# Optimization experiments

Hardware: AMD Instinct MI355X
Metric: run time of the kernel (lower is better)

The kernel has to match this reference:

```python
import jax, jax.numpy as jnp
import numpy as np

B = 64        # graphs per batch
NP = 96       # nodes per graph
H = 64        # hid_size
IN_F = 32     # node feature dim
E_F = 16      # edge feature dim
DEG = 8       # avg degree
ENSEMBLE = 1


def _lin(key, fan_in, fan_out):
    return jax.random.normal(key, (fan_in, fan_out), jnp.float32) / np.float32(np.sqrt(fan_in))


def setup_inputs() -> dict:
    key = jax.random.key(0)
    ks = jax.random.split(key, 12)
    N = B * NP
    E = B * NP * DEG
    x = jax.random.normal(ks[0], (N, IN_F), jnp.float32)
    edge_attr = jax.random.normal(ks[1], (E, E_F), jnp.float32)
    # within-graph random edges (sorted per-graph blocks, like is_sorted=True)
    rng = np.random.default_rng(0)
    off = (np.arange(B) * NP)[:, None]
    src = (rng.integers(0, NP, size=(B, NP * DEG)) + off).ravel()
    dst = (rng.integers(0, NP, size=(B, NP * DEG)) + off).ravel()
    edge_index = jnp.asarray(np.stack([src, dst]), dtype=jnp.int32)
    # idx = concat of triu_indices(n, -n) per graph == ALL n^2 pairs per graph
    tri = np.triu_indices(NP, -NP)
    idx0 = jnp.asarray((tri[0][None, :] + off).ravel(), jnp.int32)  # [B*NP^2]
    idx1 = jnp.asarray((tri[1][None, :] + off).ravel(), jnp.int32)
    params = dict(
        W_atom=_lin(ks[2], IN_F, H), b_atom=jnp.zeros((H,), jnp.float32),
        W_bond=_lin(ks[3], E_F, H), b_bond=jnp.zeros((H,), jnp.float32),
        W_node=_lin(ks[4], H, H), b_node=jnp.zeros((H,), jnp.float32),
        W_edge=_lin(ks[5], H, H), b_edge=jnp.zeros((H,), jnp.float32),
        W1=_lin(ks[6], 3 * H, H), b1=jnp.zeros((H,), jnp.float32),
        W2=_lin(ks[7], H, H), b2=jnp.zeros((H,), jnp.float32),
        W3=_lin(ks[8], H, ENSEMBLE), b3=jnp.zeros((ENSEMBLE,), jnp.float32),
    )
    return dict(x=x, edge_attr=edge_attr, edge_index=edge_index,
                idx0=idx0, idx1=idx1, n=NP, **params)


def reference(x, edge_attr, edge_index, idx0, idx1, n,
              W_atom, b_atom, W_bond, b_bond, W_node, b_node,
              W_edge, b_edge, W1, b1, W2, b2, W3, b3):
    # encoders
    xh = x @ W_atom + b_atom                 # [N, H]
    eh = edge_attr @ W_bond + b_bond         # [E, H]
    emb_n = xh @ W_node + b_node             # [N, H]
    emb_e = eh @ W_edge + b_edge             # [E, H]
    # SparseTensor.to_dense() then gather at idx == scatter-add edge embeddings
    # into the per-graph dense pairwise slot (duplicates sum, missing = 0),
    # without materializing the O(N^2) adjacency.
    u, v = edge_index[0], edge_index[1]
    g = u // n
    pair_idx = g * (n * n) + (u - g * n) * n + (v - g * n)   # [E]
    P = idx0.shape[0]                         # B * n^2, idx enumerates all pairs row-major
    pair_e = jnp.zeros((P, emb_e.shape[1]), emb_e.dtype).at[pair_idx].add(emb_e)
    emb = jnp.concatenate((emb_n[idx0], emb_n[idx1], pair_e), axis=-1)  # [P, 3H]
    # MLP [3H, H, H, ensemble], plain last layer
    h = jax.nn.relu(emb @ W1 + b1)
    h = jax.nn.relu(h @ W2 + b2)
    return h @ W3 + b3                        # [P, ensemble]
```

## Files before the change

### kernel.cpp

```cpp
#include <hip/hip_runtime.h>

#define NPG 96
#define BGR 64
#define HID 64
#define INF 32
#define EF  16
#define DEG 8
#define NN  (BGR*NPG)
#define NE  (BGR*NPG*DEG)
#define EPG (NPG*DEG)
#define PPG (NPG*NPG)
#define BMW 288

typedef short bf16x8 __attribute__((ext_vector_type(8)));
typedef float f32x4  __attribute__((ext_vector_type(4)));

__device__ __forceinline__ unsigned rne2(float lo, float hi) {
    union { float f; unsigned u; } a, b; a.f = lo; b.f = hi;
    unsigned ua = a.u + 0x7FFF + ((a.u >> 16) & 1);
    unsigned ub = b.u + 0x7FFF + ((b.u >> 16) & 1);
    return (ua >> 16) | (ub & 0xFFFF0000u);
}
__device__ __forceinline__ unsigned short rne1(float x) {
    union { float f; unsigned u; } a; a.f = x;
    return (unsigned short)((a.u + 0x7FFF + ((a.u >> 16) & 1)) >> 16);
}

__global__ __launch_bounds__(768) void prep_kernel(
    const float* __restrict__ x,
    const float* __restrict__ W_atom, const float* __restrict__ b_atom,
    const float* __restrict__ W_node, const float* __restrict__ b_node,
    const float* __restrict__ W1,     const float* __restrict__ b1,
    const float* __restrict__ ea,     const int* __restrict__ eidx,
    const float* __restrict__ W_bond, const float* __restrict__ b_bond,
    const float* __restrict__ W_edge, const float* __restrict__ b_edge,
    float* __restrict__ Abuf, float* __restrict__ Bbuf,
    int* __restrict__ fkey, int* __restrict__ fcnt,
    float* __restrict__ fsea, int* __restrict__ gcount,
    float* __restrict__ wec, float* __restrict__ biascg,
    unsigned* __restrict__ gbm)
{
    __shared__ __align__(16) char smem[45504];
    const int t = threadIdx.x;

    if (blockIdx.x >= 64) {
        float* sh = (float*)smem;
        const int wave = t >> 6, lane = t & 63;
        const int n = __builtin_amdgcn_readfirstlane((blockIdx.x - 64)*12 + wave);
        const float* xr = x + n * INF;

        float xh = b_atom[lane];
        #pragma unroll
        for (int k = 0; k < INF; ++k) xh += xr[k] * W_atom[k*HID + lane];
        sh[wave*64 + lane] = xh;
        __syncthreads();

        float en = b_node[lane];
        #pragma unroll
        for (int k = 0; k < HID; ++k) en += sh[wave*64 + k] * W_node[k*HID + lane];
        __syncthreads();
        sh[wave*64 + lane] = en;
        __syncthreads();

        float a = b1[lane], b = 0.f;
        #pragma unroll
        for (int k = 0; k < HID; ++k) {
            const float ek = sh[wave*64 + k];
            a += ek * W1[k*HID + lane];
            b += ek * W1[(HID + k)*HID + lane];
        }
        Abuf[n*HID + lane] = a;
        Bbuf[n*HID + lane] = b;
        return;
    }

    int*      head = (int*)smem;
    int*      nxt  = (int*)(smem + 36864);
    float*    sU   = (float*)(smem + 36864 + 3072);
    float*    sbe  = (float*)(smem + 36864 + 3072 + 4096);
    unsigned* bm   = (unsigned*)(smem + 36864+3072+4096+256);
    int*      lcnt = (int*)(smem + 36864+3072+4096+256+1152);
    const int g = blockIdx.x;

    for (int idx = t; idx < PPG; idx += EPG) head[idx] = -1;
    for (int idx = t; idx < BMW; idx += EPG) bm[idx] = 0u;
    if (t == 0) *lcnt = 0;

    const int u = eidx[g*EPG + t]      - g*NPG;
    const int v = eidx[NE + g*EPG + t] - g*NPG;
    const int key = u*NPG + v;
    __syncthreads();

    nxt[t] = atomicExch(&head[key], t);
    __syncthreads();

    if (head[key] == t) {
        const float* eag = ea + (size_t)g * EPG * EF;
        float s[EF];
        #pragma unroll
        for (int q = 0; q < EF; ++q) s[q] = 0.f;
        int cnt = 0;
        for (int e = t; e != -1; e = nxt[e]) {
            ++cnt;
            const float4* p = (const float4*)(eag + e*EF);
            #pragma unroll
            for (int q4 = 0; q4 < 4; ++q4) {
                const float4 f = p[q4];
                s[q4*4+0] += f.x; s[q4*4+1] += f.y;
                s[q4*4+2] += f.z; s[q4*4+3] += f.w;
            }
        }
        atomicOr(&bm[key >> 5], 1u << (key & 31));
        const int pos  = atomicAdd(lcnt, 1);
        const int slot = g*EPG + pos;
        fkey[slot] = key;
        fcnt[slot] = cnt;
        #pragma unroll
        for (int q = 0; q < EF; ++q) fsea[slot*EF + q] = s[q];
    }
    __syncthreads();
    for (int idx = t; idx < BMW; idx += EPG) gbm[g*BMW + idx] = bm[idx];
    if (t == 0) gcount[g] = *lcnt;

    if (g == 0) {
        for (int idx = t; idx < 16*64; idx += EPG) {
            const int r = idx >> 6, c = idx & 63;
            float s = 0.f;
            for (int k = 0; k < 64; ++k) s += W_bond[r*64+k] * W_edge[k*64+c];
            sU[idx] = s;
        }
        if (t < 64) {
            float s2 = b_edge[t];
            for (int k = 0; k < 64; ++k) s2 += b_bond[k] * W_edge[k*64+t];
            sbe[t] = s2;
        }
        __syncthreads();
        for (int idx = t; idx < 16*64; idx += EPG) {
            const int r = idx >> 6, c = idx & 63;
            float s = 0.f;
            for (int k = 0; k < 64; ++k) s += sU[r*64+k] * W1[(128+k)*64+c];
            wec[idx] = s;
        }
        if (t < 64) {
            float sc = 0.f;
            for (int k = 0; k < 64; ++k) sc += sbe[k] * W1[(128+k)*64+t];
            biascg[t] = sc;
        }
    }
}

#define SBST 68
#define W2ST 72
#define FIXW 16
__global__ __launch_bounds__(256) void pair_kernel(
    const float* __restrict__ Abuf, const float* __restrict__ Bbuf,
    const int* __restrict__ fkey, const int* __restrict__ fcnt,
    const float* __restrict__ fsea, const int* __restrict__ gcount,
    const float* __restrict__ wec,  const float* __restrict__ biascg,
    const unsigned* __restrict__ gbm,
    const float* __restrict__ W2,   const float* __restrict__ b2,
    const float* __restrict__ W3,   const float* __restrict__ b3,
    float* __restrict__ out)
{
    __shared__ __align__(16) char smem[37504];
    const int t = threadIdx.x;
    const int wave = t >> 6, lane = t & 63;
    const int col = lane & 15, q = lane >> 4;
    const float b3v = b3[0];

    if (blockIdx.x < 768) {
        float*          sB   = (float*)smem;
        float*          sA   = (float*)(smem + 26112);
        unsigned short* sW2t = (unsigned short*)(smem + 28160);
        unsigned*       sBM  = (unsigned*)(smem + 28160 + 9216);
        const int g  = blockIdx.x / 12;
        const int i0 = (blockIdx.x % 12) * 8;

        const float* Bg = Bbuf + g * NPG * 64;
        for (int idx = t; idx < NPG*64; idx += 256)
            sB[(idx >> 6)*SBST + (idx & 63)] = Bg[idx];
        for (int idx = t; idx < 8*64; idx += 256)
            sA[idx] = Abuf[(g*NPG + i0 + (idx >> 6))*64 + (idx & 63)];
        for (int idx = t; idx < 64*64; idx += 256) {
            const int k = idx >> 6, n = idx & 63;
            sW2t[n*W2ST + k] = rne1(W2[idx]);
        }
        if (t < 24) sBM[t] = gbm[g*BMW + i0*3 + t];
        __syncthreads();

        bf16x8 w2f[4][2];
        #pragma unroll
        for (int nt = 0; nt < 4; ++nt)
            #pragma unroll
            for (int c = 0; c < 2; ++c)
                w2f[nt][c] = *(const bf16x8*)(sW2t + (nt*16 + col)*W2ST + c*32 + q*8);

        float w3l[4], b2l[4];
        #pragma unroll
        for (int nt = 0; nt < 4; ++nt) {
            w3l[nt] = W3[nt*16 + col];
            b2l[nt] = b2[nt*16 + col];
        }

        #pragma unroll
        for (int ii = 0; ii < 2; ++ii) {
            const int il = wave*2 + ii;
            float areg[16];
            {
                const float4* Ar = (const float4*)(sA + il*64 + q*8);
                const float4 a0 = Ar[0], a1 = Ar[1];
                const float4 a2 = Ar[8], a3 = Ar[9];
                areg[0]=a0.x; areg[1]=a0.y; areg[2]=a0.z; areg[3]=a0.w;
                areg[4]=a1.x; areg[5]=a1.y; areg[6]=a1.z; areg[7]=a1.w;
                areg[8]=a2.x; areg[9]=a2.y; areg[10]=a2.z; areg[11]=a2.w;
                areg[12]=a3.x; areg[13]=a3.y; areg[14]=a3.z; areg[15]=a3.w;
            }
            float* outr = out + g*PPG + (i0 + il)*NPG;

            for (int jc = 0; jc < 6; ++jc) {
                const int j0 = jc * 16;
                union { bf16x8 v; unsigned u[4]; } h1[2];
                const float* Brow = sB + (j0 + col)*SBST + q*8;
                #pragma unroll
                for (int c = 0; c < 2; ++c) {
                    const float4 b0 = *(const float4*)(Brow + c*32);
                    const float4 b1v = *(const float4*)(Brow + c*32 + 4);
                    float h[8];
                    h[0] = fmaxf(areg[c*8+0] + b0.x, 0.f);
                    h[1] = fmaxf(areg[c*8+1] + b0.y, 0.f);
                    h[2] = fmaxf(areg[c*8+2] + b0.z, 0.f);
                    h[3] = fmaxf(areg[c*8+3] + b0.w, 0.f);
                    h[4] = fmaxf(areg[c*8+4] + b1v.x, 0.f);
                    h[5] = fmaxf(areg[c*8+5] + b1v.y, 0.f);
                    h[6] = fmaxf(areg[c*8+6] + b1v.z, 0.f);
                    h[7] = fmaxf(areg[c*8+7] + b1v.w, 0.f);
                    #pragma unroll
                    for (int p2 = 0; p2 < 4; ++p2)
                        h1[c].u[p2] = rne2(h[2*p2], h[2*p2+1]);
                }
                f32x4 acc[4];
                #pragma unroll
                for (int nt = 0; nt < 4; ++nt) {
                    f32x4 z = {0.f, 0.f, 0.f, 0.f};
                    z = __builtin_amdgcn_mfma_f32_16x16x32_bf16(h1[0].v, w2f[nt][0], z, 0, 0, 0);
                    z = __builtin_amdgcn_mfma_f32_16x16x32_bf16(h1[1].v, w2f[nt][1], z, 0, 0, 0);
                    acc[nt] = z;
                }
                float p[4];
                #pragma unroll
                for (int r = 0; r < 4; ++r) {
                    float s = 0.f;
                    #pragma unroll
                    for (int nt = 0; nt < 4; ++nt)
                        s += fmaxf(acc[nt][r] + b2l[nt], 0.f) * w3l[nt];
                    p[r] = s;
                }
                #pragma unroll
                for (int off = 1; off < 16; off <<= 1) {
                    #pragma unroll
                    for (int r = 0; r < 4; ++r)
                        p[r] += __shfl_xor(p[r], off, 64);
                }
                if (col == 0) {
                    #pragma unroll
                    for (int r = 0; r < 4; ++r) {
                        const int j = j0 + q*4 + r;
                        if (!((sBM[il*3 + (j >> 5)] >> (j & 31)) & 1u))
                            outr[j] = p[r] + b3v;
                    }
                }
            }
        }
        return;
    }

    unsigned short* sW2t = (unsigned short*)smem;
    float*          sWEc = (float*)(smem + 9216);
    float*          sbc  = (float*)(smem + 9216 + 4096);

    for (int idx = t; idx < 64*64; idx += 256) {
        const int k = idx >> 6, n = idx & 63;
        sW2t[n*W2ST + k] = rne1(W2[idx]);
    }
    for (int idx = t; idx < 16*64; idx += 256) sWEc[idx] = wec[idx];
    if (t < 64) sbc[t] = biascg[t];
    __syncthreads();

    const int fb = blockIdx.x - 768;
    const int s0 = (fb * 4 + wave) * FIXW;
    const int g  = s0 / EPG;
    const int l0 = s0 % EPG;
    const int cg = gcount[g];
    if (l0 >= cg) return;

    bf16x8 w2f[4][2];
    #pragma unroll
    for (int nt = 0; nt < 4; ++nt)
        #pragma unroll
        for (int c = 0; c < 2; ++c)
            w2f[nt][c] = *(const bf16x8*)(sW2t + (nt*16 + col)*W2ST + c*32 + q*8);

    float w3l[4], b2l[4];
    #pragma unroll
    for (int nt = 0; nt < 4; ++nt) {
        w3l[nt] = W3[nt*16 + col];
        b2l[nt] = b2[nt*16 + col];
    }
    const int k0 = q * 8;

    union { bf16x8 v; unsigned u[4]; } h1[2];
    #pragma unroll
    for (int p2 = 0; p2 < 4; ++p2) { h1[0].u[p2] = 0; h1[1].u[p2] = 0; }

    const int s = s0 + col;
    if (l0 + col < cg) {
        const int key  = fkey[s];
        const float cf = (float)fcnt[s];
        const int ui = key / NPG, vi = key % NPG;

        float se[16];
        {
            const float4* p = (const float4*)(fsea + (size_t)s * EF);
            #pragma unroll
            for (int q4 = 0; q4 < 4; ++q4) {
                const float4 f = p[q4];
                se[q4*4+0] = f.x; se[q4*4+1] = f.y;
                se[q4*4+2] = f.z; se[q4*4+3] = f.w;
            }
        }

        float ck[16];
        #pragma unroll
        for (int kk = 0; kk < 8; ++kk) {
            ck[kk]     = cf * sbc[k0 + kk];
            ck[8 + kk] = cf * sbc[32 + k0 + kk];
        }
        #pragma unroll
        for (int qq = 0; qq < 16; ++qq) {
            const float sq = se[qq];
            const float4 w0 = *(const float4*)(sWEc + qq*64 + k0);
            const float4 w1 = *(const float4*)(sWEc + qq*64 + k0 + 4);
            const float4 w2v = *(const float4*)(sWEc + qq*64 + k0 + 32);
            const float4 w3v = *(const float4*)(sWEc + qq*64 + k0 + 36);
            ck[0]  += sq * w0.x;  ck[1]  += sq * w0.y;
            ck[2]  += sq * w0.z;  ck[3]  += sq * w0.w;
            ck[4]  += sq * w1.x;  ck[5]  += sq * w1.y;
            ck[6]  += sq * w1.z;  ck[7]  += sq * w1.w;
            ck[8]  += sq * w2v.x; ck[9]  += sq * w2v.y;
            ck[10] += sq * w2v.z; ck[11] += sq * w2v.w;
            ck[12] += sq * w3v.x; ck[13] += sq * w3v.y;
            ck[14] += sq * w3v.z; ck[15] += sq * w3v.w;
        }

        const float* Ar = Abuf + (g*NPG + ui)*64;
        const float* Br = Bbuf + (g*NPG + vi)*64;
        const float4 a0 = *(const float4*)(Ar + k0);
        const float4 a1 = *(const float4*)(Ar + k0 + 4);
        const float4 a2 = *(const float4*)(Ar + k0 + 32);
        const float4 a3 = *(const float4*)(Ar + k0 + 36);
        const float4 c0 = *(const float4*)(Br + k0);
        const float4 c1 = *(const float4*)(Br + k0 + 4);
        const float4 c2 = *(const float4*)(Br + k0 + 32);
        const float4 c3 = *(const float4*)(Br + k0 + 36);

        float h[16];
        h[0]  = fmaxf(a0.x + c0.x + ck[0],  0.f);
        h[1]  = fmaxf(a0.y + c0.y + ck[1],  0.f);
        h[2]  = fmaxf(a0.z + c0.z + ck[2],  0.f);
        h[3]  = fmaxf(a0.w + c0.w + ck[3],  0.f);
        h[4]  = fmaxf(a1.x + c1.x + ck[4],  0.f);
        h[5]  = fmaxf(a1.y + c1.y + ck[5],  0.f);
        h[6]  = fmaxf(a1.z + c1.z + ck[6],  0.f);
        h[7]  = fmaxf(a1.w + c1.w + ck[7],  0.f);
        h[8]  = fmaxf(a2.x + c2.x + ck[8],  0.f);
        h[9]  = fmaxf(a2.y + c2.y + ck[9],  0.f);
        h[10] = fmaxf(a2.z + c2.z + ck[10], 0.f);
        h[11] = fmaxf(a2.w + c2.w + ck[11], 0.f);
        h[12] = fmaxf(a3.x + c3.x + ck[12], 0.f);
        h[13] = fmaxf(a3.y + c3.y + ck[13], 0.f);
        h[14] = fmaxf(a3.z + c3.z + ck[14], 0.f);
        h[15] = fmaxf(a3.w + c3.w + ck[15], 0.f);
        #pragma unroll
        for (int p2 = 0; p2 < 4; ++p2) {
            h1[0].u[p2] = rne2(h[2*p2],     h[2*p2 + 1]);
            h1[1].u[p2] = rne2(h[8 + 2*p2], h[8 + 2*p2 + 1]);
        }
    }

    f32x4 acc[4];
    #pragma unroll
    for (int nt = 0; nt < 4; ++nt) {
        f32x4 z = {0.f, 0.f, 0.f, 0.f};
        z = __builtin_amdgcn_mfma_f32_16x16x32_bf16(h1[0].v, w2f[nt][0], z, 0, 0, 0);
        z = __builtin_amdgcn_mfma_f32_16x16x32_bf16(h1[1].v, w2f[nt][1], z, 0, 0, 0);
        acc[nt] = z;
    }

    float p[4];
    #pragma unroll
    for (int r = 0; r < 4; ++r) {
        float sum = 0.f;
        #pragma unroll
        for (int nt = 0; nt < 4; ++nt)
            sum += fmaxf(acc[nt][r] + b2l[nt], 0.f) * w3l[nt];
        p[r] = sum;
    }
    #pragma unroll
    for (int off = 1; off < 16; off <<= 1) {
        #pragma unroll
        for (int r = 0; r < 4; ++r)
            p[r] += __shfl_xor(p[r], off, 64);
    }
    if (col == 0) {
        #pragma unroll
        for (int r = 0; r < 4; ++r) {
            const int lr = q*4 + r;
            if (l0 + lr < cg) {
                const int keyr = fkey[s0 + lr];
                out[g*PPG + keyr] = p[r] + b3v;
            }
        }
    }
}

extern "C" void kernel_launch(void* const* d_in, const int* in_sizes, int n_in,
                              void* d_out, int out_size, void* d_ws, size_t ws_size,
                              hipStream_t stream)
{
    const float* x      = (const float*)d_in[0];
    const float* ea     = (const float*)d_in[1];
    const int*   eidx   = (const int*)  d_in[2];
    const float* W_atom = (const float*)d_in[6];
    const float* b_atom = (const float*)d_in[7];
    const float* W_bond = (const float*)d_in[8];
    const float* b_bond = (const float*)d_in[9];
    const float* W_node = (const float*)d_in[10];
    const float* b_node = (const float*)d_in[11];
    const float* W_edge = (const float*)d_in[12];
    const float* b_edge = (const float*)d_in[13];
    const float* W1     = (const float*)d_in[14];
    const float* b1     = (const float*)d_in[15];
    const float* W2     = (const float*)d_in[16];
    const float* b2     = (const float*)d_in[17];
    const float* W3     = (const float*)d_in[18];
    const float* b3     = (const float*)d_in[19];
    float* out = (float*)d_out;

    float* ws    = (float*)d_ws;
    float* Abuf  = ws;
    float* Bbuf  = Abuf  + NN*HID;
    float* fsea  = Bbuf  + NN*HID;
    int*   fkey  = (int*)(fsea + NE*EF);
    int*   fcnt  = fkey + NE;
    int*   gcount= fcnt + NE;
    float* wec   = (float*)(gcount + BGR);
    float* biascg= wec + 16*64;
    unsigned* gbm= (unsigned*)(biascg + 64);

    prep_kernel<<<64 + NN/12, 768, 0, stream>>>(
        x, W_atom, b_atom, W_node, b_node, W1, b1,
        ea, eidx, W_bond, b_bond, W_edge, b_edge,
        Abuf, Bbuf, fkey, fcnt, fsea, gcount, wec, biascg, gbm);
    pair_kernel<<<768 + NE/(FIXW*4), 256, 0, stream>>>(
        Abuf, Bbuf, fkey, fcnt, fsea, gcount, wec, biascg, gbm,
        W2, b2, W3, b3, out);
}
```

Baseline: 142.4 us.

## Retile pair kernel, precompute bf16 W2 once, batch node prep and fixups

```diff
diff --git a/kernel.cpp b/kernel.cpp
--- a/kernel.cpp
+++ b/kernel.cpp
@@ -1,4 +1,8 @@
 #include <hip/hip_runtime.h>
+#if __has_include(<hip/hip_bf16.h>)
+#include <hip/hip_bf16.h>
+#define HAVE_BF16_H 1
+#endif
 
 #define NPG 96
 #define BGR 64
@@ -11,6 +15,9 @@
 #define EPG (NPG*DEG)
 #define PPG (NPG*NPG)
 #define BMW 288
+#define W2ST 72
+#define SBST 68
+#define FIXW 16
 
 typedef short bf16x8 __attribute__((ext_vector_type(8)));
 typedef float f32x4  __attribute__((ext_vector_type(4)));
@@ -25,6 +32,14 @@
     union { float f; unsigned u; } a; a.f = x;
     return (unsigned short)((a.u + 0x7FFF + ((a.u >> 16) & 1)) >> 16);
 }
+__device__ __forceinline__ unsigned cvt2(float lo, float hi) {
+#ifdef HAVE_BF16_H
+    __hip_bfloat162 h2 = __float22bfloat162_rn(make_float2(lo, hi));
+    unsigned u; __builtin_memcpy(&u, &h2, 4); return u;
+#else
+    return rne2(lo, hi);
+#endif
+}
 
 __global__ __launch_bounds__(768) void prep_kernel(
     const float* __restrict__ x,
@@ -34,43 +49,48 @@
     const float* __restrict__ ea,     const int* __restrict__ eidx,
     const float* __restrict__ W_bond, const float* __restrict__ b_bond,
     const float* __restrict__ W_edge, const float* __restrict__ b_edge,
+    const float* __restrict__ W2,
     float* __restrict__ Abuf, float* __restrict__ Bbuf,
     int* __restrict__ fkey, int* __restrict__ fcnt,
     float* __restrict__ fsea, int* __restrict__ gcount,
     float* __restrict__ wec, float* __restrict__ biascg,
-    unsigned* __restrict__ gbm)
+    unsigned* __restrict__ gbm, unsigned short* __restrict__ w2bf)
 {
     __shared__ __align__(16) char smem[45504];
     const int t = threadIdx.x;
 
     if (blockIdx.x >= 64) {
-        float* sh = (float*)smem;
         const int wave = t >> 6, lane = t & 63;
-        const int n = __builtin_amdgcn_readfirstlane((blockIdx.x - 64)*12 + wave);
-        const float* xr = x + n * INF;
-
-        float xh = b_atom[lane];
-        #pragma unroll
-        for (int k = 0; k < INF; ++k) xh += xr[k] * W_atom[k*HID + lane];
-        sh[wave*64 + lane] = xh;
-        __syncthreads();
-
-        float en = b_node[lane];
-        #pragma unroll
-        for (int k = 0; k < HID; ++k) en += sh[wave*64 + k] * W_node[k*HID + lane];
-        __syncthreads();
-        sh[wave*64 + lane] = en;
-        __syncthreads();
-
-        float a = b1[lane], b = 0.f;
+        const int nb = __builtin_amdgcn_readfirstlane((blockIdx.x - 64)*12 + wave);
+        const float* xr0 = x + (size_t)(2*nb) * INF;
+
+        float xh0 = b_atom[lane], xh1 = xh0;
+        #pragma unroll
+        for (int k = 0; k < INF; ++k) {
+            const float w = W_atom[k*HID + lane];
+            xh0 += xr0[k] * w;
+            xh1 += xr0[INF + k] * w;
+        }
+        float en0 = b_node[lane], en1 = en0;
         #pragma unroll
         for (int k = 0; k < HID; ++k) {
-            const float ek = sh[wave*64 + k];
-            a += ek * W1[k*HID + lane];
-            b += ek * W1[(HID + k)*HID + lane];
-        }
-        Abuf[n*HID + lane] = a;
-        Bbuf[n*HID + lane] = b;
+            const float w = W_node[k*HID + lane];
+            en0 += __shfl(xh0, k) * w;
+            en1 += __shfl(xh1, k) * w;
+        }
+        float a0 = b1[lane], a1 = a0, bb0 = 0.f, bb1 = 0.f;
+        #pragma unroll
+        for (int k = 0; k < HID; ++k) {
+            const float w1a = W1[k*HID + lane];
+            const float w1b = W1[(HID + k)*HID + lane];
+            const float e0 = __shfl(en0, k), e1 = __shfl(en1, k);
+            a0  += e0 * w1a;  a1  += e1 * w1a;
+            bb0 += e0 * w1b;  bb1 += e1 * w1b;
+        }
+        Abuf[(2*nb    )*HID + lane] = a0;
+        Abuf[(2*nb + 1)*HID + lane] = a1;
+        Bbuf[(2*nb    )*HID + lane] = bb0;
+        Bbuf[(2*nb + 1)*HID + lane] = bb1;
         return;
     }
 
@@ -82,7 +102,10 @@
     int*      lcnt = (int*)(smem + 36864+3072+4096+256+1152);
     const int g = blockIdx.x;
 
-    for (int idx = t; idx < PPG; idx += EPG) head[idx] = -1;
+    {
+        int4* h4 = (int4*)head;
+        for (int idx = t; idx < PPG/4; idx += EPG) h4[idx] = make_int4(-1,-1,-1,-1);
+    }
     for (int idx = t; idx < BMW; idx += EPG) bm[idx] = 0u;
     if (t == 0) *lcnt = 0;
 
@@ -123,6 +146,14 @@
     if (t == 0) gcount[g] = *lcnt;
 
     if (g == 0) {
+        for (int idx = t; idx < 64*64; idx += EPG) {
+            const int k = idx >> 6, n = idx & 63;
+            w2bf[n*W2ST + k] = rne1(W2[idx]);
+        }
+        for (int idx = t; idx < 64*8; idx += EPG) {
+            const int n = idx >> 3, kk = 64 + (idx & 7);
+            w2bf[n*W2ST + kk] = 0;
+        }
         for (int idx = t; idx < 16*64; idx += EPG) {
             const int r = idx >> 6, c = idx & 63;
             float s = 0.f;
@@ -149,20 +180,17 @@
     }
 }
 
-#define SBST 68
-#define W2ST 72
-#define FIXW 16
 __global__ __launch_bounds__(256) void pair_kernel(
     const float* __restrict__ Abuf, const float* __restrict__ Bbuf,
     const int* __restrict__ fkey, const int* __restrict__ fcnt,
     const float* __restrict__ fsea, const int* __restrict__ gcount,
     const float* __restrict__ wec,  const float* __restrict__ biascg,
-    const unsigned* __restrict__ gbm,
-    const float* __restrict__ W2,   const float* __restrict__ b2,
+    const unsigned* __restrict__ gbm, const unsigned short* __restrict__ w2bf,
+    const float* __restrict__ b2,
     const float* __restrict__ W3,   const float* __restrict__ b3,
     float* __restrict__ out)
 {
-    __shared__ __align__(16) char smem[37504];
+    __shared__ __align__(16) char smem[26560];
     const int t = threadIdx.x;
     const int wave = t >> 6, lane = t & 63;
     const int col = lane & 15, q = lane >> 4;
@@ -170,22 +198,26 @@
 
     if (blockIdx.x < 768) {
         float*          sB   = (float*)smem;
-        float*          sA   = (float*)(smem + 26112);
-        unsigned short* sW2t = (unsigned short*)(smem + 28160);
-        unsigned*       sBM  = (unsigned*)(smem + 28160 + 9216);
-        const int g  = blockIdx.x / 12;
-        const int i0 = (blockIdx.x % 12) * 8;
-
-        const float* Bg = Bbuf + g * NPG * 64;
-        for (int idx = t; idx < NPG*64; idx += 256)
+        float*          sA   = (float*)(smem + 13056);
+        unsigned short* sW2t = (unsigned short*)(smem + 17152);
+        unsigned*       sBM  = (unsigned*)(smem + 26368);
+        const int db = blockIdx.x;
+        const int g  = db / 12;
+        const int rm = db % 12;
+        const int i0 = (rm >> 1) * 16;
+        const int jb = (rm & 1) * 48;
+
+        const float* Bg = Bbuf + (g*NPG + jb) * HID;
+        for (int idx = t; idx < 48*64; idx += 256)
             sB[(idx >> 6)*SBST + (idx & 63)] = Bg[idx];
-        for (int idx = t; idx < 8*64; idx += 256)
-            sA[idx] = Abuf[(g*NPG + i0 + (idx >> 6))*64 + (idx & 63)];
-        for (int idx = t; idx < 64*64; idx += 256) {
-            const int k = idx >> 6, n = idx & 63;
-            sW2t[n*W2ST + k] = rne1(W2[idx]);
-        }
-        if (t < 24) sBM[t] = gbm[g*BMW + i0*3 + t];
+        for (int idx = t; idx < 16*64; idx += 256)
+            sA[idx] = Abuf[(g*NPG + i0 + (idx >> 6))*HID + (idx & 63)];
+        {
+            const uint4* src = (const uint4*)w2bf;
+            uint4* dst = (uint4*)sW2t;
+            for (int idx = t; idx < 576; idx += 256) dst[idx] = src[idx];
+        }
+        if (t < 48) sBM[t] = gbm[g*BMW + i0*3 + t];
         __syncthreads();
 
         bf16x8 w2f[4][2];
@@ -203,8 +235,8 @@
         }
 
         #pragma unroll
-        for (int ii = 0; ii < 2; ++ii) {
-            const int il = wave*2 + ii;
+        for (int ii = 0; ii < 4; ++ii) {
+            const int il = wave*4 + ii;
             float areg[16];
             {
                 const float4* Ar = (const float4*)(sA + il*64 + q*8);
@@ -217,7 +249,7 @@
             }
             float* outr = out + g*PPG + (i0 + il)*NPG;
 
-            for (int jc = 0; jc < 6; ++jc) {
+            for (int jc = 0; jc < 3; ++jc) {
                 const int j0 = jc * 16;
                 union { bf16x8 v; unsigned u[4]; } h1[2];
                 const float* Brow = sB + (j0 + col)*SBST + q*8;
@@ -236,7 +268,7 @@
                     h[7] = fmaxf(areg[c*8+7] + b1v.w, 0.f);
                     #pragma unroll
                     for (int p2 = 0; p2 < 4; ++p2)
-                        h1[c].u[p2] = rne2(h[2*p2], h[2*p2+1]);
+                        h1[c].u[p2] = cvt2(h[2*p2], h[2*p2+1]);
                 }
                 f32x4 acc[4];
                 #pragma unroll
@@ -261,13 +293,14 @@
                     for (int r = 0; r < 4; ++r)
                         p[r] += __shfl_xor(p[r], off, 64);
                 }
-                if (col == 0) {
-                    #pragma unroll
-                    for (int r = 0; r < 4; ++r) {
-                        const int j = j0 + q*4 + r;
-                        if (!((sBM[il*3 + (j >> 5)] >> (j & 31)) & 1u))
-                            outr[j] = p[r] + b3v;
-                    }
+                if (col < 4) {
+                    const int j = jb + j0 + q*4 + col;
+                    float pv = p[0];
+                    pv = (col == 1) ? p[1] : pv;
+                    pv = (col == 2) ? p[2] : pv;
+                    pv = (col == 3) ? p[3] : pv;
+                    if (!((sBM[il*3 + (j >> 5)] >> (j & 31)) & 1u))
+                        outr[j] = pv + b3v;
                 }
             }
         }
@@ -278,20 +311,14 @@
     float*          sWEc = (float*)(smem + 9216);
     float*          sbc  = (float*)(smem + 9216 + 4096);
 
-    for (int idx = t; idx < 64*64; idx += 256) {
-        const int k = idx >> 6, n = idx & 63;
-        sW2t[n*W2ST + k] = rne1(W2[idx]);
+    {
+        const uint4* src = (const uint4*)w2bf;
+        uint4* dst = (uint4*)sW2t;
+        for (int idx = t; idx < 576; idx += 256) dst[idx] = src[idx];
     }
     for (int idx = t; idx < 16*64; idx += 256) sWEc[idx] = wec[idx];
     if (t < 64) sbc[t] = biascg[t];
     __syncthreads();
-
-    const int fb = blockIdx.x - 768;
-    const int s0 = (fb * 4 + wave) * FIXW;
-    const int g  = s0 / EPG;
-    const int l0 = s0 % EPG;
-    const int cg = gcount[g];
-    if (l0 >= cg) return;
 
     bf16x8 w2f[4][2];
     #pragma unroll
@@ -307,117 +334,127 @@
         b2l[nt] = b2[nt*16 + col];
     }
     const int k0 = q * 8;
-
-    union { bf16x8 v; unsigned u[4]; } h1[2];
-    #pragma unroll
-    for (int p2 = 0; p2 < 4; ++p2) { h1[0].u[p2] = 0; h1[1].u[p2] = 0; }
-
-    const int s = s0 + col;
-    if (l0 + col < cg) {
-        const int key  = fkey[s];
-        const float cf = (float)fcnt[s];
-        const int ui = key / NPG, vi = key % NPG;
-
-        float se[16];
-        {
-            const float4* p = (const float4*)(fsea + (size_t)s * EF);
-            #pragma unroll
-            for (int q4 = 0; q4 < 4; ++q4) {
-                const float4 f = p[q4];
-                se[q4*4+0] = f.x; se[q4*4+1] = f.y;
-                se[q4*4+2] = f.z; se[q4*4+3] = f.w;
-            }
-        }
-
-        float ck[16];
-        #pragma unroll
-        for (int kk = 0; kk < 8; ++kk) {
-            ck[kk]     = cf * sbc[k0 + kk];
-            ck[8 + kk] = cf * sbc[32 + k0 + kk];
-        }
-        #pragma unroll
-        for (int qq = 0; qq < 16; ++qq) {
-            const float sq = se[qq];
-            const float4 w0 = *(const float4*)(sWEc + qq*64 + k0);
-            const float4 w1 = *(const float4*)(sWEc + qq*64 + k0 + 4);
-            const float4 w2v = *(const float4*)(sWEc + qq*64 + k0 + 32);
-            const float4 w3v = *(const float4*)(sWEc + qq*64 + k0 + 36);
-            ck[0]  += sq * w0.x;  ck[1]  += sq * w0.y;
-            ck[2]  += sq * w0.z;  ck[3]  += sq * w0.w;
-            ck[4]  += sq * w1.x;  ck[5]  += sq * w1.y;
-            ck[6]  += sq * w1.z;  ck[7]  += sq * w1.w;
-            ck[8]  += sq * w2v.x; ck[9]  += sq * w2v.y;
-            ck[10] += sq * w2v.z; ck[11] += sq * w2v.w;
-            ck[12] += sq * w3v.x; ck[13] += sq * w3v.y;
-            ck[14] += sq * w3v.z; ck[15] += sq * w3v.w;
-        }
-
-        const float* Ar = Abuf + (g*NPG + ui)*64;
-        const float* Br = Bbuf + (g*NPG + vi)*64;
-        const float4 a0 = *(const float4*)(Ar + k0);
-        const float4 a1 = *(const float4*)(Ar + k0 + 4);
-        const float4 a2 = *(const float4*)(Ar + k0 + 32);
-        const float4 a3 = *(const float4*)(Ar + k0 + 36);
-        const float4 c0 = *(const float4*)(Br + k0);
-        const float4 c1 = *(const float4*)(Br + k0 + 4);
-        const float4 c2 = *(const float4*)(Br + k0 + 32);
-        const float4 c3 = *(const float4*)(Br + k0 + 36);
-
-        float h[16];
-        h[0]  = fmaxf(a0.x + c0.x + ck[0],  0.f);
-        h[1]  = fmaxf(a0.y + c0.y + ck[1],  0.f);
-        h[2]  = fmaxf(a0.z + c0.z + ck[2],  0.f);
-        h[3]  = fmaxf(a0.w + c0.w + ck[3],  0.f);
-        h[4]  = fmaxf(a1.x + c1.x + ck[4],  0.f);
-        h[5]  = fmaxf(a1.y + c1.y + ck[5],  0.f);
-        h[6]  = fmaxf(a1.z + c1.z + ck[6],  0.f);
-        h[7]  = fmaxf(a1.w + c1.w + ck[7],  0.f);
-        h[8]  = fmaxf(a2.x + c2.x + ck[8],  0.f);
-        h[9]  = fmaxf(a2.y + c2.y + ck[9],  0.f);
-        h[10] = fmaxf(a2.z + c2.z + ck[10], 0.f);
-        h[11] = fmaxf(a2.w + c2.w + ck[11], 0.f);
-        h[12] = fmaxf(a3.x + c3.x + ck[12], 0.f);
-        h[13] = fmaxf(a3.y + c3.y + ck[13], 0.f);
-        h[14] = fmaxf(a3.z + c3.z + ck[14], 0.f);
-        h[15] = fmaxf(a3.w + c3.w + ck[15], 0.f);
-        #pragma unroll
-        for (int p2 = 0; p2 < 4; ++p2) {
-            h1[0].u[p2] = rne2(h[2*p2],     h[2*p2 + 1]);
-            h1[1].u[p2] = rne2(h[8 + 2*p2], h[8 + 2*p2 + 1]);
-        }
-    }
-
-    f32x4 acc[4];
-    #pragma unroll
-    for (int nt = 0; nt < 4; ++nt) {
-        f32x4 z = {0.f, 0.f, 0.f, 0.f};
-        z = __builtin_amdgcn_mfma_f32_16x16x32_bf16(h1[0].v, w2f[nt][0], z, 0, 0, 0);
-        z = __builtin_amdgcn_mfma_f32_16x16x32_bf16(h1[1].v, w2f[nt][1], z, 0, 0, 0);
-        acc[nt] = z;
-    }
-
-    float p[4];
-    #pragma unroll
-    for (int r = 0; r < 4; ++r) {
-        float sum = 0.f;
-        #pragma unroll
-        for (int nt = 0; nt < 4; ++nt)
-            sum += fmaxf(acc[nt][r] + b2l[nt], 0.f) * w3l[nt];
-        p[r] = sum;
-    }
-    #pragma unroll
-    for (int off = 1; off < 16; off <<= 1) {
-        #pragma unroll
-        for (int r = 0; r < 4; ++r)
-            p[r] += __shfl_xor(p[r], off, 64);
-    }
-    if (col == 0) {
+    const int fb = blockIdx.x - 768;
+
+    for (int it = 0; it < 3; ++it) {
+        const int ch = fb*12 + wave*3 + it;
+        const int s0 = ch * FIXW;
+        const int g  = s0 / EPG;
+        const int l0 = s0 % EPG;
+        const int cg = gcount[g];
+        if (l0 >= cg) continue;
+
+        union { bf16x8 v; unsigned u[4]; } h1[2];
+        #pragma unroll
+        for (int p2 = 0; p2 < 4; ++p2) { h1[0].u[p2] = 0; h1[1].u[p2] = 0; }
+
+        const int s = s0 + col;
+        if (l0 + col < cg) {
+            const int key  = fkey[s];
+            const float cf = (float)fcnt[s];
+            const int ui = key / NPG, vi = key % NPG;
+
+            float se[16];
+            {
+                const float4* p = (const float4*)(fsea + (size_t)s * EF);
+                #pragma unroll
+                for (int q4 = 0; q4 < 4; ++q4) {
+                    const float4 f = p[q4];
+                    se[q4*4+0] = f.x; se[q4*4+1] = f.y;
+                    se[q4*4+2] = f.z; se[q4*4+3] = f.w;
+                }
+            }
+
+            float ck[16];
+            #pragma unroll
+            for (int kk = 0; kk < 8; ++kk) {
+                ck[kk]     = cf * sbc[k0 + kk];
+                ck[8 + kk] = cf * sbc[32 + k0 + kk];
+            }
+            #pragma unroll
+            for (int qq = 0; qq < 16; ++qq) {
+                const float sq = se[qq];
+                const float4 w0 = *(const float4*)(sWEc + qq*64 + k0);
+                const float4 w1 = *(const float4*)(sWEc + qq*64 + k0 + 4);
+                const float4 w2v = *(const float4*)(sWEc + qq*64 + k0 + 32);
+                const float4 w3v = *(const float4*)(sWEc + qq*64 + k0 + 36);
+                ck[0]  += sq * w0.x;  ck[1]  += sq * w0.y;
+                ck[2]  += sq * w0.z;  ck[3]  += sq * w0.w;
+                ck[4]  += sq * w1.x;  ck[5]  += sq * w1.y;
+                ck[6]  += sq * w1.z;  ck[7]  += sq * w1.w;
+                ck[8]  += sq * w2v.x; ck[9]  += sq * w2v.y;
+                ck[10] += sq * w2v.z; ck[11] += sq * w2v.w;
+                ck[12] += sq * w3v.x; ck[13] += sq * w3v.y;
+                ck[14] += sq * w3v.z; ck[15] += sq * w3v.w;
+            }
+
+            const float* Ar = Abuf + (g*NPG + ui)*64;
+            const float* Br = Bbuf + (g*NPG + vi)*64;
+            const float4 a0 = *(const float4*)(Ar + k0);
+            const float4 a1 = *(const float4*)(Ar + k0 + 4);
+            const float4 a2 = *(const float4*)(Ar + k0 + 32);
+            const float4 a3 = *(const float4*)(Ar + k0 + 36);
+            const float4 c0 = *(const float4*)(Br + k0);
+            const float4 c1 = *(const float4*)(Br + k0 + 4);
+            const float4 c2 = *(const float4*)(Br + k0 + 32);
+            const float4 c3 = *(const float4*)(Br + k0 + 36);
+
+            float h[16];
+            h[0]  = fmaxf(a0.x + c0.x + ck[0],  0.f);
+            h[1]  = fmaxf(a0.y + c0.y + ck[1],  0.f);
+            h[2]  = fmaxf(a0.z + c0.z + ck[2],  0.f);
+            h[3]  = fmaxf(a0.w + c0.w + ck[3],  0.f);
+            h[4]  = fmaxf(a1.x + c1.x + ck[4],  0.f);
+            h[5]  = fmaxf(a1.y + c1.y + ck[5],  0.f);
+            h[6]  = fmaxf(a1.z + c1.z + ck[6],  0.f);
+            h[7]  = fmaxf(a1.w + c1.w + ck[7],  0.f);
+            h[8]  = fmaxf(a2.x + c2.x + ck[8],  0.f);
+            h[9]  = fmaxf(a2.y + c2.y + ck[9],  0.f);
+            h[10] = fmaxf(a2.z + c2.z + ck[10], 0.f);
+            h[11] = fmaxf(a2.w + c2.w + ck[11], 0.f);
+            h[12] = fmaxf(a3.x + c3.x + ck[12], 0.f);
+            h[13] = fmaxf(a3.y + c3.y + ck[13], 0.f);
+            h[14] = fmaxf(a3.z + c3.z + ck[14], 0.f);
+            h[15] = fmaxf(a3.w + c3.w + ck[15], 0.f);
+            #pragma unroll
+            for (int p2 = 0; p2 < 4; ++p2) {
+                h1[0].u[p2] = cvt2(h[2*p2],     h[2*p2 + 1]);
+                h1[1].u[p2] = cvt2(h[8 + 2*p2], h[8 + 2*p2 + 1]);
+            }
+        }
+
+        f32x4 acc[4];
+        #pragma unroll
+        for (int nt = 0; nt < 4; ++nt) {
+            f32x4 z = {0.f, 0.f, 0.f, 0.f};
+            z = __builtin_amdgcn_mfma_f32_16x16x32_bf16(h1[0].v, w2f[nt][0], z, 0, 0, 0);
+            z = __builtin_amdgcn_mfma_f32_16x16x32_bf16(h1[1].v, w2f[nt][1], z, 0, 0, 0);
+            acc[nt] = z;
+        }
+
+        float p[4];
         #pragma unroll
         for (int r = 0; r < 4; ++r) {
-            const int lr = q*4 + r;
+            float sum = 0.f;
+            #pragma unroll
+            for (int nt = 0; nt < 4; ++nt)
+                sum += fmaxf(acc[nt][r] + b2l[nt], 0.f) * w3l[nt];
+            p[r] = sum;
+        }
+        #pragma unroll
+        for (int off = 1; off < 16; off <<= 1) {
+            #pragma unroll
+            for (int r = 0; r < 4; ++r)
+                p[r] += __shfl_xor(p[r], off, 64);
+        }
+        if (col < 4) {
+            const int lr = q*4 + col;
             if (l0 + lr < cg) {
-                const int keyr = fkey[s0 + lr];
-                out[g*PPG + keyr] = p[r] + b3v;
+                float pv = p[0];
+                pv = (col == 1) ? p[1] : pv;
+                pv = (col == 2) ? p[2] : pv;
+                pv = (col == 3) ? p[3] : pv;
+                out[g*PPG + fkey[s0 + lr]] = pv + b3v;
             }
         }
     }
@@ -456,12 +493,13 @@
     float* wec   = (float*)(gcount + BGR);
     float* biascg= wec + 16*64;
     unsigned* gbm= (unsigned*)(biascg + 64);
-
-    prep_kernel<<<64 + NN/12, 768, 0, stream>>>(
+    unsigned short* w2bf = (unsigned short*)(gbm + BGR*BMW);
+
+    prep_kernel<<<64 + NN/24, 768, 0, stream>>>(
         x, W_atom, b_atom, W_node, b_node, W1, b1,
-        ea, eidx, W_bond, b_bond, W_edge, b_edge,
-        Abuf, Bbuf, fkey, fcnt, fsea, gcount, wec, biascg, gbm);
-    pair_kernel<<<768 + NE/(FIXW*4), 256, 0, stream>>>(
-        Abuf, Bbuf, fkey, fcnt, fsea, gcount, wec, biascg, gbm,
-        W2, b2, W3, b3, out);
+        ea, eidx, W_bond, b_bond, W_edge, b_edge, W2,
+        Abuf, Bbuf, fkey, fcnt, fsea, gcount, wec, biascg, gbm, w2bf);
+    pair_kernel<<<768 + 256, 256, 0, stream>>>(
+        Abuf, Bbuf, fkey, fcnt, fsea, gcount, wec, biascg, gbm, w2bf,
+        b2, W3, b3, out);
 }
```

After: 155.9 us. 9.5% more time.
